# Kernel tuning notes

Measured on AMD Instinct MI355X. Metric: run time of the kernel, lower is better.

## Reference

```python
import jax, jax.numpy as jnp
import numpy as np

C = 512
GROUPS = 32
EPS = 1e-5  # torch GroupNorm default


def setup_inputs() -> dict:
    key = jax.random.key(0)
    ks = jax.random.split(key, 11)
    B, H, W = 4, 64, 64
    s = 1.0 / np.sqrt(C)
    inp = {
        "x": jax.random.normal(ks[0], (B, C, H, W), dtype=jnp.float32),
        "gn_scale": jnp.ones((C,), jnp.float32),
        "gn_bias": jnp.zeros((C,), jnp.float32),
        "wq": jax.random.normal(ks[1], (C, C), jnp.float32) * s,
        "bq": jax.random.normal(ks[2], (C,), jnp.float32) * 0.01,
        "wk": jax.random.normal(ks[3], (C, C), jnp.float32) * s,
        "bk": jax.random.normal(ks[4], (C,), jnp.float32) * 0.01,
        "wv": jax.random.normal(ks[5], (C, C), jnp.float32) * s,
        "bv": jax.random.normal(ks[6], (C,), jnp.float32) * 0.01,
        "wo": jax.random.normal(ks[7], (C, C), jnp.float32) * s,
        "bo": jax.random.normal(ks[8], (C,), jnp.float32) * 0.01,
    }
    return inp


def group_norm(x, scale, bias):
    # x: [B, C, H, W]; normalize within each of GROUPS channel groups over (C/G, H, W)
    B, Cc, H, W = x.shape
    xg = x.reshape(B, GROUPS, Cc // GROUPS, H, W)
    mean = jnp.mean(xg, axis=(2, 3, 4), keepdims=True)
    var = jnp.var(xg, axis=(2, 3, 4), keepdims=True)
    xg = (xg - mean) * jax.lax.rsqrt(var + EPS)
    xn = xg.reshape(B, Cc, H, W)
    return xn * scale[None, :, None, None] + bias[None, :, None, None]


def reference(x, gn_scale, gn_bias, wq, bq, wk, bk, wv, bv, wo, bo):
    B, Cc, H, W = x.shape
    h = group_norm(x, gn_scale, gn_bias)
    # 1x1 convs == channel matmuls; work in [B, HW, C] layout
    hf = h.reshape(B, Cc, H * W).transpose(0, 2, 1)  # [B, N, C]
    q = hf @ wq.T + bq                               # [B, N, C]
    k = hf @ wk.T + bk
    v = hf @ wv.T + bv
    scale = jnp.asarray(Cc, x.dtype) ** -0.5
    attn = jnp.einsum("bnc,bmc->bnm", q, k) * scale  # [B, N, N]
    attn = jax.nn.softmax(attn, axis=-1)
    o = jnp.einsum("bnm,bmc->bnc", attn, v)          # [B, N, C]
    o = o @ wo.T + bo
    o = o.transpose(0, 2, 1).reshape(B, Cc, H, W)
    return x + o
```

## Files before the change

kernel.cpp:

```cpp
#include <hip/hip_runtime.h>
#include <cstdint>
#include <cstddef>

typedef unsigned short ushort_t;
typedef __attribute__((ext_vector_type(8))) __bf16 bf16x8;
typedef __attribute__((ext_vector_type(4))) float f32x4;

#define DEVINL __device__ __forceinline__

DEVINL ushort_t f2bf(float f) {
  union { float f; unsigned u; } v; v.f = f;
  unsigned r = (v.u + 0x7fffu + ((v.u >> 16) & 1u)) >> 16;
  return (ushort_t)r;
}
DEVINL float bf2f(ushort_t u) {
  union { unsigned u; float f; } v; v.u = ((unsigned)u) << 16;
  return v.f;
}

DEVINL float wred_sum(float x) {
#pragma unroll
  for (int o = 32; o > 0; o >>= 1) x += __shfl_xor(x, o, 64);
  return x;
}

DEVINL void async16(ushort_t* lds, const ushort_t* g) {
  __builtin_amdgcn_global_load_lds(
      (__attribute__((address_space(1))) const unsigned int*)g,
      (__attribute__((address_space(3))) unsigned int*)lds, 16, 0, 0);
}

template <int CPR>
DEVINL int fswz(int r) {
  if constexpr (CPR == 4) return (r >> 2) & 3;
  else return r & 7;
}

__global__ __launch_bounds__(256) void gn_stats_k(const float* __restrict__ x,
                                                  float* __restrict__ stats) {
  const int bg = blockIdx.x;
  const float4* base = (const float4*)(x + ((size_t)bg << 16));
  float s = 0.f, q = 0.f;
  for (int i = threadIdx.x; i < 16384; i += 256) {
    float4 f = base[i];
    s += f.x + f.y + f.z + f.w;
    q += f.x * f.x + f.y * f.y + f.z * f.z + f.w * f.w;
  }
  s = wred_sum(s);
  q = wred_sum(q);
  __shared__ float rs[4], rq[4];
  const int lane = threadIdx.x & 63, wid = threadIdx.x >> 6;
  if (lane == 0) { rs[wid] = s; rq[wid] = q; }
  __syncthreads();
  if (threadIdx.x == 0) {
    float S = rs[0] + rs[1] + rs[2] + rs[3];
    float Q = rq[0] + rq[1] + rq[2] + rq[3];
    float mean = S * (1.f / 65536.f);
    float var = Q * (1.f / 65536.f) - mean * mean;
    stats[2 * bg] = mean;
    stats[2 * bg + 1] = rsqrtf(var + 1e-5f);
  }
}

__global__ __launch_bounds__(256) void gn_apply_k(const float* __restrict__ x,
                                                  const float* __restrict__ stats,
                                                  const float* __restrict__ gs,
                                                  const float* __restrict__ gb,
                                                  ushort_t* __restrict__ h) {
  __shared__ ushort_t tile[32][33];
  const int bid = blockIdx.x;
  const int b = bid >> 11;
  const int r = bid & 2047;
  const int ct = r >> 7, nt = r & 127;
  const int c0 = ct << 5, n0 = nt << 5;
  const int tx = threadIdx.x & 31, ty = threadIdx.x >> 5;
#pragma unroll
  for (int i = 0; i < 4; ++i) {
    const int c = c0 + ty + i * 8;
    const float mean = stats[2 * (b * 32 + (c >> 4))];
    const float rstd = stats[2 * (b * 32 + (c >> 4)) + 1];
    const float xv = x[(((size_t)b * 512 + c) << 12) + n0 + tx];
    tile[ty + i * 8][tx] = f2bf((xv - mean) * rstd * gs[c] + gb[c]);
  }
  __syncthreads();
#pragma unroll
  for (int i = 0; i < 4; ++i) {
    const int n = n0 + ty + i * 8;
    h[(((size_t)b << 12) + n) * 512 + c0 + tx] = tile[tx][ty + i * 8];
  }
}

struct Ptr4 { const float* src[4]; float wsc[4]; };
__global__ __launch_bounds__(256) void cvt_all_k(Ptr4 s, ushort_t* __restrict__ dst) {
  const int i = blockIdx.x * 256 + threadIdx.x;
  const int m = i >> 18;
  dst[i] = f2bf(s.src[m][i & 262143] * s.wsc[m]);
}

struct Ptr3 { const float* bias[3]; ushort_t* out[3]; float bs[3]; };

template <int BM, int BN, int BK, int EPI>
__global__ __launch_bounds__(256) void gemm_nt_k(
    const ushort_t* __restrict__ A, int lda, const ushort_t* __restrict__ Bm, int ldb,
    void* __restrict__ Cout, int ldc, const float* __restrict__ bias,
    const float* __restrict__ resid, float scale, int K,
    size_t azs, size_t bzs, size_t czs, Ptr3 p3, float* __restrict__ lbuf) {
  constexpr int CPR = BK / 8;
  constexpr int WTM = BM / 2, WTN = BN / 2;
  constexpr int MI = WTM / 16, NI = WTN / 16;
  constexpr int AR = (BM * CPR) / 256;
  constexpr int BR = (BN * CPR) / 256;
  __shared__ ushort_t Als[BM * BK];
  __shared__ ushort_t Bls[BN * BK];
  const int tid = threadIdx.x;
  const int lane = tid & 63;
  const int wid = tid >> 6;
  const int quad = lane >> 4;
  const int r16 = lane & 15;
  const int wm = wid >> 1, wn = wid & 1;
  const int m0 = blockIdx.y * BM;
  const int n0 = blockIdx.x * BN;
  const int zb = blockIdx.z;

  A += azs * zb;
  Bm += bzs * zb;

  f32x4 acc[MI][NI] = {};

  for (int kt = 0; kt < K; kt += BK) {
#pragma unroll
    for (int r = 0; r < AR; ++r) {
      const int s = r * 256 + tid;
      const int row = s / CPR;
      const int q = (s % CPR) ^ fswz<CPR>(row);
      async16(&Als[s << 3], A + (size_t)(m0 + row) * lda + kt + (q << 3));
    }
#pragma unroll
    for (int r = 0; r < BR; ++r) {
      const int s = r * 256 + tid;
      const int row = s / CPR;
      const int q = (s % CPR) ^ fswz<CPR>(row);
      async16(&Bls[s << 3], Bm + (size_t)(n0 + row) * ldb + kt + (q << 3));
    }
    __syncthreads();
#pragma unroll
    for (int kf = 0; kf < BK / 32; ++kf) {
      bf16x8 af[MI], bfr[NI];
#pragma unroll
      for (int mi = 0; mi < MI; ++mi) {
        const int lr = wm * WTM + mi * 16 + r16;
        const int ch = kf * 4 + quad;
        af[mi] = *reinterpret_cast<const bf16x8*>(
            &Als[(lr * CPR + (ch ^ fswz<CPR>(lr))) << 3]);
      }
#pragma unroll
      for (int ni = 0; ni < NI; ++ni) {
        const int lr = wn * WTN + ni * 16 + r16;
        const int ch = kf * 4 + quad;
        bfr[ni] = *reinterpret_cast<const bf16x8*>(
            &Bls[(lr * CPR + (ch ^ fswz<CPR>(lr))) << 3]);
      }
#pragma unroll
      for (int mi = 0; mi < MI; ++mi)
#pragma unroll
        for (int ni = 0; ni < NI; ++ni)
          acc[mi][ni] = __builtin_amdgcn_mfma_f32_16x16x32_bf16(
              af[mi], bfr[ni], acc[mi][ni], 0, 0, 0);
    }
    __syncthreads();
  }

  const int mrow = m0 + wm * WTM;
  const int ncol = n0 + wn * WTN;
  if constexpr (EPI == 2) {
    float* C = (float*)Cout;
#pragma unroll
    for (int ni = 0; ni < NI; ++ni) {
      const int col = ncol + ni * 16 + r16;
      const float bvv = bias[col];
#pragma unroll
      for (int mi = 0; mi < MI; ++mi) {
        const int rowb = mrow + mi * 16 + quad * 4;
        const int bb = rowb >> 12;
        const int nl = rowb & 4095;
        const size_t base = (((size_t)bb * 512 + col) << 12) + nl;
        const float4 rv = *(const float4*)&resid[base];
        float4 ov;
        ov.x = rv.x + acc[mi][ni][0] + bvv;
        ov.y = rv.y + acc[mi][ni][1] + bvv;
        ov.z = rv.z + acc[mi][ni][2] + bvv;
        ov.w = rv.w + acc[mi][ni][3] + bvv;
        *(float4*)&C[base] = ov;
      }
    }
  } else if constexpr (EPI == 3) {
    const float* bz = p3.bias[zb];
    const float bsc = p3.bs[zb];
    ushort_t* O = p3.out[zb];
    if (zb < 2) {
#pragma unroll
      for (int ni = 0; ni < NI; ++ni) {
        const int col = ncol + ni * 16 + r16;
        const float bvv = bz[col] * bsc;
#pragma unroll
        for (int mi = 0; mi < MI; ++mi) {
          const int rowb = mrow + mi * 16 + quad * 4;
#pragma unroll
          for (int rr = 0; rr < 4; ++rr)
            O[(size_t)(rowb + rr) * 512 + col] = f2bf(acc[mi][ni][rr] + bvv);
        }
      }
    } else {
#pragma unroll
      for (int ni = 0; ni < NI; ++ni) {
        const int col = ncol + ni * 16 + r16;
        const float bvv = bz[col];
#pragma unroll
        for (int mi = 0; mi < MI; ++mi) {
          const int rowb = mrow + mi * 16 + quad * 4;
          const int bb = rowb >> 12;
          const int nn = rowb & 4095;
          ushort4 pk;
          pk.x = f2bf(acc[mi][ni][0] + bvv);
          pk.y = f2bf(acc[mi][ni][1] + bvv);
          pk.z = f2bf(acc[mi][ni][2] + bvv);
          pk.w = f2bf(acc[mi][ni][3] + bvv);
          *(ushort4*)&O[(((size_t)bb * 512 + col) << 12) + nn] = pk;
        }
      }
    }
  } else if constexpr (EPI == 4) {
    ushort_t* C = (ushort_t*)Cout + czs * zb;
    float* Lz = lbuf + (size_t)zb * 4096;
#pragma unroll
    for (int mi = 0; mi < MI; ++mi) {
#pragma unroll
      for (int rr = 0; rr < 4; ++rr) {
        const int row = mrow + mi * 16 + quad * 4 + rr;
        float ps = 0.f;
#pragma unroll
        for (int ni = 0; ni < NI; ++ni) {
          const int col = ncol + ni * 16 + r16;
          const ushort_t ub = f2bf(__expf(acc[mi][ni][rr]));
          C[(size_t)row * ldc + col] = ub;
          ps += bf2f(ub);
        }
#pragma unroll
        for (int o = 1; o < 16; o <<= 1) ps += __shfl_xor(ps, o, 64);
        if (r16 == 0) atomicAdd(&Lz[row], ps);
      }
    }
  } else {
    ushort_t* C = (ushort_t*)Cout + czs * zb;
    const float* Lz = lbuf + (size_t)zb * 4096;
#pragma unroll
    for (int mi = 0; mi < MI; ++mi) {
#pragma unroll
      for (int rr = 0; rr < 4; ++rr) {
        const int row = mrow + mi * 16 + quad * 4 + rr;
        const float inv = 1.f / Lz[row];
#pragma unroll
        for (int ni = 0; ni < NI; ++ni) {
          const int col = ncol + ni * 16 + r16;
          C[(size_t)row * ldc + col] = f2bf(acc[mi][ni][rr] * inv);
        }
      }
    }
  }
}

extern "C" void kernel_launch(void* const* d_in, const int* in_sizes, int n_in,
                              void* d_out, int out_size, void* d_ws, size_t ws_size,
                              hipStream_t stream) {
  const float* x  = (const float*)d_in[0];
  const float* gs = (const float*)d_in[1];
  const float* gb = (const float*)d_in[2];
  const float* wq = (const float*)d_in[3];
  const float* bq = (const float*)d_in[4];
  const float* wk = (const float*)d_in[5];
  const float* bk = (const float*)d_in[6];
  const float* wv = (const float*)d_in[7];
  const float* bv = (const float*)d_in[8];
  const float* wo = (const float*)d_in[9];
  const float* bo = (const float*)d_in[10];
  float* out = (float*)d_out;

  const size_t HNC = (size_t)4 * 4096 * 512;
  char* w = (char*)d_ws;
  float* stats  = (float*)w;    w += 4096;
  float* Ls     = (float*)w;    w += (size_t)4 * 4096 * 4;
  ushort_t* wb  = (ushort_t*)w; w += (size_t)4 * 262144 * 2;
  ushort_t* h   = (ushort_t*)w; w += HNC * 2;
  ushort_t* q   = (ushort_t*)w; w += HNC * 2;
  ushort_t* kk  = (ushort_t*)w; w += HNC * 2;
  ushort_t* vt  = (ushort_t*)w; w += HNC * 2;
  ushort_t* Se  = (ushort_t*)w; w += (size_t)4 * 4096 * 4096 * 2;

  const float sc = 0.044194173824159216f;

  gn_stats_k<<<128, 256, 0, stream>>>(x, stats);
  gn_apply_k<<<8192, 256, 0, stream>>>(x, stats, gs, gb, h);
  Ptr4 wsrc;
  wsrc.src[0] = wq; wsrc.src[1] = wk; wsrc.src[2] = wv; wsrc.src[3] = wo;
  wsrc.wsc[0] = sc; wsrc.wsc[1] = 1.f; wsrc.wsc[2] = 1.f; wsrc.wsc[3] = 1.f;
  cvt_all_k<<<4096, 256, 0, stream>>>(wsrc, wb);
  hipMemsetAsync(Ls, 0, (size_t)4 * 4096 * 4, stream);

  Ptr3 qkv;
  qkv.bias[0] = bq; qkv.bias[1] = bk; qkv.bias[2] = bv;
  qkv.out[0] = q; qkv.out[1] = kk; qkv.out[2] = vt;
  qkv.bs[0] = sc; qkv.bs[1] = 1.f; qkv.bs[2] = 1.f;
  gemm_nt_k<128, 128, 32, 3><<<dim3(4, 128, 3), 256, 0, stream>>>(
      h, 512, wb, 512, nullptr, 0, nullptr, nullptr, 1.f, 512,
      0, 262144, 0, qkv, nullptr);

  Ptr3 e0{};
  gemm_nt_k<128, 128, 64, 4><<<dim3(32, 32, 4), 256, 0, stream>>>(
      q, 512, kk, 512, Se, 4096, nullptr, nullptr, 1.f, 512,
      (size_t)4096 * 512, (size_t)4096 * 512, (size_t)4096 * 4096, e0, Ls);
  gemm_nt_k<128, 128, 64, 5><<<dim3(4, 32, 4), 256, 0, stream>>>(
      Se, 4096, vt, 4096, h, 512, nullptr, nullptr, 1.f, 4096,
      (size_t)4096 * 4096, (size_t)512 * 4096, (size_t)4096 * 512, e0, Ls);

  gemm_nt_k<128, 128, 32, 2><<<dim3(4, 128, 1), 256, 0, stream>>>(
      h, 512, wb + (size_t)3 * 262144, 512, out, 512, bo, x, 1.f, 512,
      0, 0, 0, e0, nullptr);
}
```

Measured before the change: 406.7 us.

## Add 512-thread 256-row GEMM with 4-stage async LDS pipeline for attention

Replaces the two attention GEMMs (QK^T with exp epilogue and PV with normalization) with a new 512-thread kernel using 256xBN tiles. It adds a 4-slot async global-to-LDS ring buffer with XOR swizzle, s_setprio around the MFMA block, and opts into large dynamic shared memory. It also swaps the manual float-to-bf16 rounding for the native __bf16 conversion. The aim is more data reuse per block and better overlap of loads with MFMA, at the cost of heavy LDS use (up to 128KB), which limits occupancy.

```diff
diff --git a/kernel.cpp b/kernel.cpp
--- a/kernel.cpp
+++ b/kernel.cpp
@@ -9,9 +9,9 @@
 #define DEVINL __device__ __forceinline__
 
 DEVINL ushort_t f2bf(float f) {
-  union { float f; unsigned u; } v; v.f = f;
-  unsigned r = (v.u + 0x7fffu + ((v.u >> 16) & 1u)) >> 16;
-  return (ushort_t)r;
+  union { __bf16 b; ushort_t u; } v;
+  v.b = (__bf16)f;
+  return v.u;
 }
 DEVINL float bf2f(ushort_t u) {
   union { unsigned u; float f; } v; v.u = ((unsigned)u) << 16;
@@ -35,6 +35,8 @@
   if constexpr (CPR == 4) return (r >> 2) & 3;
   else return r & 7;
 }
+
+DEVINL int hswz(int r) { return (r & 3) ^ ((r >> 2) & 3); }
 
 __global__ __launch_bounds__(256) void gn_stats_k(const float* __restrict__ x,
                                                   float* __restrict__ stats) {
@@ -229,7 +231,106 @@
         }
       }
     }
-  } else if constexpr (EPI == 4) {
+  }
+}
+
+template <int BN, int EPI>
+__global__ __launch_bounds__(512) void gemm8_nt_k(
+    const ushort_t* __restrict__ A, int lda,
+    const ushort_t* __restrict__ Bm, int ldb,
+    void* __restrict__ Cout, int ldc, int K,
+    size_t azs, size_t bzs, size_t czs,
+    float* __restrict__ lbuf) {
+  constexpr int WGN = BN / 64;
+  constexpr int WGM = 8 / WGN;
+  constexpr int WTM = 256 / WGM;
+  constexpr int WTN = BN / WGN;
+  constexpr int MI = WTM / 16;
+  constexpr int NI = WTN / 16;
+  constexpr int ASZ = 256 * 32;
+  constexpr int BSZ = BN * 32;
+  constexpr int BLD = BN / 128;
+  constexpr int VMC = (2 + BLD) * 2;
+
+  extern __shared__ ushort_t lds8[];
+  const int tid = threadIdx.x;
+  const int lane = tid & 63;
+  const int wid = tid >> 6;
+  const int quad = lane >> 4;
+  const int r16 = lane & 15;
+  const int wm = wid / WGN, wn = wid % WGN;
+  const int m0 = blockIdx.y * 256;
+  const int n0 = blockIdx.x * BN;
+  const int zb = blockIdx.z;
+
+  A += azs * zb;
+  Bm += bzs * zb;
+
+  const int NPH = K >> 5;
+
+  f32x4 acc[MI][NI] = {};
+
+  auto stage = [&](int ph) {
+    const int php = ph < NPH ? ph : NPH - 1;
+    const int kt = (php >> 1) << 6;
+    const int kf = php & 1;
+    const int slot = ph & 3;
+    ushort_t* As = lds8 + slot * ASZ;
+    ushort_t* Bs = lds8 + 4 * ASZ + slot * BSZ;
+#pragma unroll
+    for (int r = 0; r < 2; ++r) {
+      const int s = r * 512 + tid;
+      const int row = s >> 2, c = s & 3;
+      const int koff = kf * 32 + ((c ^ hswz(row)) << 3);
+      async16(&As[s << 3], A + (size_t)(m0 + row) * lda + kt + koff);
+    }
+#pragma unroll
+    for (int r = 0; r < BLD; ++r) {
+      const int s = r * 512 + tid;
+      const int row = s >> 2, c = s & 3;
+      const int koff = kf * 32 + ((c ^ hswz(row)) << 3);
+      async16(&Bs[s << 3], Bm + (size_t)(n0 + row) * ldb + kt + koff);
+    }
+  };
+
+  stage(0); stage(1); stage(2);
+
+#pragma unroll 4
+  for (int phi = 0; phi < NPH; ++phi) {
+    asm volatile("s_waitcnt vmcnt(%0)" :: "i"(VMC) : "memory");
+    __builtin_amdgcn_s_barrier();
+    stage(phi + 3);
+
+    const int slot = phi & 3;
+    const ushort_t* As = lds8 + slot * ASZ;
+    const ushort_t* Bs = lds8 + 4 * ASZ + slot * BSZ;
+    bf16x8 af[MI], bfr[NI];
+#pragma unroll
+    for (int mi = 0; mi < MI; ++mi) {
+      const int lr = wm * WTM + mi * 16 + r16;
+      const int cc = quad ^ hswz(lr);
+      af[mi] = *reinterpret_cast<const bf16x8*>(&As[((lr << 2) | cc) << 3]);
+    }
+#pragma unroll
+    for (int ni = 0; ni < NI; ++ni) {
+      const int lr = wn * WTN + ni * 16 + r16;
+      const int cc = quad ^ hswz(lr);
+      bfr[ni] = *reinterpret_cast<const bf16x8*>(&Bs[((lr << 2) | cc) << 3]);
+    }
+    __builtin_amdgcn_s_setprio(1);
+#pragma unroll
+    for (int mi = 0; mi < MI; ++mi)
+#pragma unroll
+      for (int ni = 0; ni < NI; ++ni)
+        acc[mi][ni] = __builtin_amdgcn_mfma_f32_16x16x32_bf16(
+            af[mi], bfr[ni], acc[mi][ni], 0, 0, 0);
+    __builtin_amdgcn_s_setprio(0);
+    asm volatile("s_waitcnt lgkmcnt(0)" ::: "memory");
+  }
+
+  const int mrow = m0 + wm * WTM;
+  const int ncol = n0 + wn * WTN;
+  if constexpr (EPI == 4) {
     ushort_t* C = (ushort_t*)Cout + czs * zb;
     float* Lz = lbuf + (size_t)zb * 4096;
 #pragma unroll
@@ -298,6 +399,15 @@
 
   const float sc = 0.044194173824159216f;
 
+  static bool attr_done = false;
+  if (!attr_done) {
+    (void)hipFuncSetAttribute((const void*)gemm8_nt_k<256, 4>,
+                              hipFuncAttributeMaxDynamicSharedMemorySize, 131072);
+    (void)hipFuncSetAttribute((const void*)gemm8_nt_k<128, 5>,
+                              hipFuncAttributeMaxDynamicSharedMemorySize, 131072);
+    attr_done = true;
+  }
+
   gn_stats_k<<<128, 256, 0, stream>>>(x, stats);
   gn_apply_k<<<8192, 256, 0, stream>>>(x, stats, gs, gb, h);
   Ptr4 wsrc;
@@ -314,14 +424,14 @@
       h, 512, wb, 512, nullptr, 0, nullptr, nullptr, 1.f, 512,
       0, 262144, 0, qkv, nullptr);
 
+  gemm8_nt_k<256, 4><<<dim3(16, 16, 4), 512, 131072, stream>>>(
+      q, 512, kk, 512, Se, 4096, 512,
+      (size_t)4096 * 512, (size_t)4096 * 512, (size_t)4096 * 4096, Ls);
+  gemm8_nt_k<128, 5><<<dim3(4, 16, 4), 512, 98304, stream>>>(
+      Se, 4096, vt, 4096, h, 512, 4096,
+      (size_t)4096 * 4096, (size_t)512 * 4096, (size_t)4096 * 512, Ls);
+
   Ptr3 e0{};
-  gemm_nt_k<128, 128, 64, 4><<<dim3(32, 32, 4), 256, 0, stream>>>(
-      q, 512, kk, 512, Se, 4096, nullptr, nullptr, 1.f, 512,
-      (size_t)4096 * 512, (size_t)4096 * 512, (size_t)4096 * 4096, e0, Ls);
-  gemm_nt_k<128, 128, 64, 5><<<dim3(4, 32, 4), 256, 0, stream>>>(
-      Se, 4096, vt, 4096, h, 512, nullptr, nullptr, 1.f, 4096,
-      (size_t)4096 * 4096, (size_t)512 * 4096, (size_t)4096 * 512, e0, Ls);
-
   gemm_nt_k<128, 128, 32, 2><<<dim3(4, 128, 1), 256, 0, stream>>>(
       h, 512, wb + (size_t)3 * 262144, 512, out, 512, bo, x, 1.f, 512,
       0, 0, 0, e0, nullptr);
```

Result: slower. 463.7 us (+14.0%).

## Add 8-wave ping-pong GEMM kernel for QK^T and PV attention stages

Applied to the files above, without the earlier changes.

Adds a new 512-thread GEMM kernel with larger 256-wide tiles, double-buffered LDS staging through async global-to-LDS loads, and quarter-split MFMA phases interleaved with staged prefetches. It also adds an XCD-aware block remap. The two attention GEMMs (exp-score and PV) now use this kernel in place of the generic one. This is meant to raise MFMA utilisation and hide memory latency on the dominant N×N stages, at the cost of large dynamic shared memory and fewer resident blocks. The bf16 conversion is also switched to the compiler's native cast.

```diff
diff --git a/kernel.cpp b/kernel.cpp
--- a/kernel.cpp
+++ b/kernel.cpp
@@ -9,9 +9,9 @@
 #define DEVINL __device__ __forceinline__
 
 DEVINL ushort_t f2bf(float f) {
-  union { float f; unsigned u; } v; v.f = f;
-  unsigned r = (v.u + 0x7fffu + ((v.u >> 16) & 1u)) >> 16;
-  return (ushort_t)r;
+  union { __bf16 b; ushort_t u; } v;
+  v.b = (__bf16)f;
+  return v.u;
 }
 DEVINL float bf2f(ushort_t u) {
   union { unsigned u; float f; } v; v.u = ((unsigned)u) << 16;
@@ -229,7 +229,145 @@
         }
       }
     }
-  } else if constexpr (EPI == 4) {
+  }
+}
+
+template <int BM, int BN, int WGM, int WGN, int EPI>
+__global__ __launch_bounds__(512, 2) void gemm8p_k(
+    const ushort_t* __restrict__ A, int lda,
+    const ushort_t* __restrict__ Bm, int ldb,
+    void* __restrict__ Cout, int ldc, int K,
+    size_t azs, size_t bzs, size_t czs, float* __restrict__ lbuf) {
+  constexpr int WTM = BM / WGM, WTN = BN / WGN;
+  constexpr int MI = WTM / 16, NI = WTN / 16;
+  constexpr int MH = MI / 2, NH = NI / 2;
+  constexpr int ALD = BM / 64;
+  constexpr int BLD = BN / 64;
+  constexpr int TOT = ALD + BLD;
+  constexpr int VMC = TOT / 4;
+  constexpr int AHALF = BM * 64;
+  constexpr int HALF = (BM + BN) * 64;
+
+  extern __shared__ ushort_t lds8[];
+  const int tid = threadIdx.x;
+  const int lane = tid & 63;
+  const int quad = lane >> 4;
+  const int r16 = lane & 15;
+  const int wid = tid >> 6;
+  const int wm = wid / WGN, wn = wid % WGN;
+
+  int bx, by, bz;
+  {
+    const int flat = blockIdx.x + (EPI == 4 ? 16 : 4) * (blockIdx.y + 16 * blockIdx.z);
+    if constexpr (EPI == 4) {
+      const int xcd = flat & 7, s = flat >> 3;
+      const int w = s & 31, half = w >> 4, idx = w & 15;
+      bx = (xcd & 3) * 4 + (idx & 3);
+      by = ((xcd >> 2) + 2 * half) * 4 + (idx >> 2);
+      bz = s >> 5;
+    } else {
+      const int xcd = flat & 7, s = flat >> 3;
+      bx = s & 3;
+      const int yz = xcd + (s >> 2) * 8;
+      by = yz & 15; bz = yz >> 4;
+    }
+  }
+  const int m0 = by * BM, n0 = bx * BN, zb = bz;
+  A += azs * zb;
+  Bm += bzs * zb;
+  const int NT = K >> 6;
+
+  const ushort_t* src[TOT];
+  ushort_t* dst[TOT];
+#pragma unroll
+  for (int l = 0; l < TOT; ++l) {
+    const bool isA = l < ALD;
+    const int li = isA ? l : l - ALD;
+    const int s = li * 512 + tid;
+    const int row = s >> 3;
+    const int q = (s & 7) ^ (row & 7);
+    src[l] = (isA ? A + (size_t)(m0 + row) * lda
+                  : Bm + (size_t)(n0 + row) * ldb) + (q << 3);
+    dst[l] = lds8 + (isA ? 0 : AHALF) + (s << 3);
+  }
+
+  f32x4 acc[MI][NI] = {};
+
+#pragma unroll
+  for (int l = 0; l < TOT; ++l) async16(dst[l], src[l]);
+
+  bf16x8 afq[MH][2], bfq[NH][2];
+
+#pragma unroll 2
+  for (int t = 0; t < NT; ++t) {
+    const int nbuf = (t + 1) & 1;
+    const ushort_t* Ab = lds8 + (t & 1) * HALF;
+    const ushort_t* Bb = Ab + AHALF;
+    const int koff = ((t + 1 < NT) ? t + 1 : NT - 1) << 6;
+
+#define STAGEG(G)                                                              \
+    { constexpr int S_ = ((G) * TOT) / 4, E_ = (((G) + 1) * TOT) / 4;          \
+      _Pragma("unroll")                                                        \
+      for (int l = S_; l < E_; ++l) async16(dst[l] + nbuf * HALF, src[l] + koff); }
+
+#define LOADA(MHh)                                                             \
+    _Pragma("unroll") for (int i = 0; i < MH; ++i)                             \
+    _Pragma("unroll") for (int kf = 0; kf < 2; ++kf) {                         \
+      const int lr = wm * WTM + ((MHh) * MH + i) * 16 + r16;                   \
+      const int cc = (kf * 4 + quad) ^ (lr & 7);                               \
+      afq[i][kf] = *reinterpret_cast<const bf16x8*>(&Ab[lr * 64 + cc * 8]); }
+
+#define LOADB(NHh)                                                             \
+    _Pragma("unroll") for (int j = 0; j < NH; ++j)                             \
+    _Pragma("unroll") for (int kf = 0; kf < 2; ++kf) {                         \
+      const int lr = wn * WTN + ((NHh) * NH + j) * 16 + r16;                   \
+      const int cc = (kf * 4 + quad) ^ (lr & 7);                               \
+      bfq[j][kf] = *reinterpret_cast<const bf16x8*>(&Bb[lr * 64 + cc * 8]); }
+
+#define MMAQ(MHh, NHh)                                                         \
+    __builtin_amdgcn_s_setprio(1);                                             \
+    _Pragma("unroll") for (int i = 0; i < MH; ++i)                             \
+    _Pragma("unroll") for (int j = 0; j < NH; ++j)                             \
+    _Pragma("unroll") for (int kf = 0; kf < 2; ++kf)                           \
+      acc[(MHh) * MH + i][(NHh) * NH + j] =                                    \
+          __builtin_amdgcn_mfma_f32_16x16x32_bf16(                             \
+              afq[i][kf], bfq[j][kf], acc[(MHh) * MH + i][(NHh) * NH + j],     \
+              0, 0, 0);                                                        \
+    __builtin_amdgcn_s_setprio(0);
+
+    STAGEG(0)
+    asm volatile("s_waitcnt vmcnt(%0)" :: "i"(VMC) : "memory");
+    __builtin_amdgcn_s_barrier();
+    __builtin_amdgcn_sched_barrier(0);
+    LOADA(0)
+    LOADB(0)
+    MMAQ(0, 0)
+    __builtin_amdgcn_sched_barrier(0);
+    __builtin_amdgcn_s_barrier();
+    STAGEG(1)
+    LOADB(1)
+    MMAQ(0, 1)
+    __builtin_amdgcn_sched_barrier(0);
+    __builtin_amdgcn_s_barrier();
+    STAGEG(2)
+    LOADA(1)
+    MMAQ(1, 1)
+    __builtin_amdgcn_sched_barrier(0);
+    __builtin_amdgcn_s_barrier();
+    STAGEG(3)
+    LOADB(0)
+    MMAQ(1, 0)
+    __builtin_amdgcn_sched_barrier(0);
+    __builtin_amdgcn_s_barrier();
+#undef STAGEG
+#undef LOADA
+#undef LOADB
+#undef MMAQ
+  }
+
+  const int mrow = m0 + wm * WTM;
+  const int ncol = n0 + wn * WTN;
+  if constexpr (EPI == 4) {
     ushort_t* C = (ushort_t*)Cout + czs * zb;
     float* Lz = lbuf + (size_t)zb * 4096;
 #pragma unroll
@@ -298,6 +436,15 @@
 
   const float sc = 0.044194173824159216f;
 
+  static bool attr_done = false;
+  if (!attr_done) {
+    (void)hipFuncSetAttribute((const void*)gemm8p_k<256, 256, 2, 4, 4>,
+                              hipFuncAttributeMaxDynamicSharedMemorySize, 131072);
+    (void)hipFuncSetAttribute((const void*)gemm8p_k<256, 128, 4, 2, 5>,
+                              hipFuncAttributeMaxDynamicSharedMemorySize, 98304);
+    attr_done = true;
+  }
+
   gn_stats_k<<<128, 256, 0, stream>>>(x, stats);
   gn_apply_k<<<8192, 256, 0, stream>>>(x, stats, gs, gb, h);
   Ptr4 wsrc;
@@ -314,14 +461,14 @@
       h, 512, wb, 512, nullptr, 0, nullptr, nullptr, 1.f, 512,
       0, 262144, 0, qkv, nullptr);
 
+  gemm8p_k<256, 256, 2, 4, 4><<<dim3(16, 16, 4), 512, 131072, stream>>>(
+      q, 512, kk, 512, Se, 4096, 512,
+      (size_t)4096 * 512, (size_t)4096 * 512, (size_t)4096 * 4096, Ls);
+  gemm8p_k<256, 128, 4, 2, 5><<<dim3(4, 16, 4), 512, 98304, stream>>>(
+      Se, 4096, vt, 4096, h, 512, 4096,
+      (size_t)4096 * 4096, (size_t)512 * 4096, (size_t)4096 * 512, Ls);
+
   Ptr3 e0{};
-  gemm_nt_k<128, 128, 64, 4><<<dim3(32, 32, 4), 256, 0, stream>>>(
-      q, 512, kk, 512, Se, 4096, nullptr, nullptr, 1.f, 512,
-      (size_t)4096 * 512, (size_t)4096 * 512, (size_t)4096 * 4096, e0, Ls);
-  gemm_nt_k<128, 128, 64, 5><<<dim3(4, 32, 4), 256, 0, stream>>>(
-      Se, 4096, vt, 4096, h, 512, nullptr, nullptr, 1.f, 4096,
-      (size_t)4096 * 4096, (size_t)512 * 4096, (size_t)4096 * 512, e0, Ls);
-
   gemm_nt_k<128, 128, 32, 2><<<dim3(4, 128, 1), 256, 0, stream>>>(
       h, 512, wb + (size_t)3 * 262144, 512, out, 512, bo, x, 1.f, 512,
       0, 0, 0, e0, nullptr);
```

After: 394.7 us. 1.03x faster.
